# Kernel optimization log

Measured on AMD Instinct MI355X. Metric: run time of the kernel, lower is better.

## Reference

```python
import jax, jax.numpy as jnp
import numpy as np

N, L, G = 8192, 120, 256          # sentences, seq_len, bags
V, P = 80000, 202                 # word vocab, position vocab
WDIM, FDIM = 50, 5                # word_size, feature_size (width = 50+2*5 = 60)
D, C = 230, 53                    # cnn_layers, num_classes


def setup_inputs() -> dict:
    key = jax.random.key(0)
    ks = jax.random.split(key, 9)
    x = jax.random.randint(ks[0], (N, L), 0, V, dtype=jnp.int32)
    ldist = jax.random.randint(ks[1], (N, L), 0, P, dtype=jnp.int32)
    rdist = jax.random.randint(ks[2], (N, L), 0, P, dtype=jnp.int32)
    # cumulative bag boundaries: 256 equal bags of 32 sentences
    total_shape = (jnp.arange(G + 1, dtype=jnp.int32) * (N // G))
    Wv = jax.random.normal(ks[3], (V, WDIM), dtype=jnp.float32) * 0.1
    pf1 = jax.random.normal(ks[4], (P, FDIM), dtype=jnp.float32) * 0.1
    pf2 = jax.random.normal(ks[5], (P, FDIM), dtype=jnp.float32) * 0.1
    Wc = jax.random.normal(ks[6], (D, 1, 3, WDIM + 2 * FDIM), dtype=jnp.float32) * 0.05
    bc = jnp.zeros((D,), dtype=jnp.float32)
    Wr = jax.random.normal(ks[7], (C, D), dtype=jnp.float32) * 0.05
    br = jnp.zeros((C,), dtype=jnp.float32)
    return dict(x=x, ldist=ldist, rdist=rdist, total_shape=total_shape,
                Wv=Wv, pf1=pf1, pf2=pf2, Wc=Wc, bc=bc, Wr=Wr, br=br)


def reference(x, ldist, rdist, total_shape, Wv, pf1, pf2, Wc, bc, Wr, br):
    n = x.shape[0]
    g = total_shape.shape[0] - 1
    # getEmbeddings: concat word + two position embeddings -> (N, L, 60)
    emb = jnp.concatenate([Wv[x], pf1[ldist], pf2[rdist]], axis=-1)
    # Conv2d(1, D, (3, 60)), VALID -> (N, D, L-2, 1)
    conv = jax.lax.conv_general_dilated(
        emb[:, None, :, :], Wc, window_strides=(1, 1), padding='VALID',
        dimension_numbers=('NCHW', 'OIHW', 'NCHW')) + bc[None, :, None, None]
    # max over positions, squeeze; dropout is identity at eval; tanh
    sent = jnp.tanh(jnp.max(conv, axis=2)[:, :, 0])           # (N, D)
    e = sent @ Wr.T + br                                       # (N, C) batch_e
    # ragged per-bag softmax over sentences (per class), honoring total_shape
    seg = jnp.searchsorted(total_shape, jnp.arange(n), side='right') - 1  # (N,)
    m = jax.ops.segment_max(e, seg, num_segments=g)            # (G, C)
    ex = jnp.exp(e - m[seg])
    den = jax.ops.segment_sum(ex, seg, num_segments=g)
    alpha = ex / den[seg]                                      # (N, C)
    # bag_rep[g, c, :] = sum_i alpha[i, c] * sent[i, :]
    bag = jax.ops.segment_sum(alpha[:, :, None] * sent[:, None, :], seg,
                              num_segments=g)                  # (G, C, D)
    scores = jnp.einsum('gcd,kd->gck', bag, Wr) + br           # (G, C, C)
    probs = jax.nn.softmax(scores, axis=-1)
    return jnp.diagonal(probs, axis1=1, axis2=2)               # (G, C)
```

## Files before the change

kernel.cpp:

```cpp
#include <hip/hip_runtime.h>
#include <hip/hip_bf16.h>

typedef __bf16 bf16x8 __attribute__((ext_vector_type(8)));
typedef float f32x16 __attribute__((ext_vector_type(16)));
typedef unsigned short ushort_t;

#define NSENT 8192
#define LSEQ  120
#define GBAGS 256
#define WDIM_ 50
#define DFILT 230
#define NCLS  53
#define KSTEPS 12
#define BFRAG_ELEMS (24*256*8)
#define SPB 8
#define CH_STRIDE 2080
#define SENT_IMG  16640

#define OFF_BFRAG 0
#define OFF_WV64  196608
#define OFF_PF1B  (OFF_WV64 + 10240000)
#define OFF_PF2B  (OFF_PF1B + 2048)
#define OFF_SENT  (OFF_PF2B + 2048)
#define OFF_TAIL  (OFF_SENT + 7536640)

static __device__ __forceinline__ ushort_t f2bf(float f) {
    unsigned int u = __float_as_uint(f);
    unsigned int lsb = (u >> 16) & 1u;
    u += 0x7fffu + lsb;
    return (ushort_t)(u >> 16);
}

__global__ __launch_bounds__(256) void pcnn_prep_b(const float* __restrict__ Wc,
                                                   const float* __restrict__ pf1,
                                                   const float* __restrict__ pf2,
                                                   ushort_t* __restrict__ Bfrag,
                                                   ushort_t* __restrict__ pf1b,
                                                   ushort_t* __restrict__ pf2b) {
    int idx = blockIdx.x * 256 + threadIdx.x;
    if (idx < 1010) pf1b[idx] = f2bf(pf1[idx]);
    else if (idx < 2020) pf2b[idx - 1010] = f2bf(pf2[idx - 1010]);
    if (idx >= BFRAG_ELEMS) return;
    int c   = idx >> 11;
    int rem = idx & 2047;
    int d   = rem >> 3;
    int j   = rem & 7;
    int k   = c * 8 + j;
    int dh  = k >> 6;
    int w   = k & 63;
    float val = (d < DFILT && w < 60) ? Wc[(d * 3 + dh) * 60 + w] : 0.0f;
    Bfrag[idx] = f2bf(val);
}

__global__ __launch_bounds__(256) void pcnn_prep_wv(const float* __restrict__ Wv,
                                                    ushort_t* __restrict__ Wv64) {
    int idx = blockIdx.x * 256 + threadIdx.x;
    int r = idx >> 6, k = idx & 63;
    float val = (k < WDIM_) ? Wv[r * WDIM_ + k] : 0.0f;
    Wv64[idx] = f2bf(val);
}

__global__ __launch_bounds__(256) void pcnn_prep_tail(
    const int* __restrict__ x, const int* __restrict__ ld, const int* __restrict__ rd,
    const ushort_t* __restrict__ Wv64, const ushort_t* __restrict__ pf1b,
    const ushort_t* __restrict__ pf2b, ushort_t* __restrict__ TailT) {
    int idx = blockIdx.x * 256 + threadIdx.x;
    if (idx >= NSENT * LSEQ) return;
    int tok = x[idx], lp = ld[idx], rp = rd[idx];
    ushort_t u[16];
    *reinterpret_cast<unsigned int*>(&u[0]) =
        *reinterpret_cast<const unsigned int*>(Wv64 + (size_t)tok * 64 + 48);
    u[2] = pf1b[lp * 5 + 0]; u[3] = pf1b[lp * 5 + 1]; u[4] = pf1b[lp * 5 + 2];
    u[5] = pf1b[lp * 5 + 3]; u[6] = pf1b[lp * 5 + 4];
    u[7] = pf2b[rp * 5 + 0];
    u[8] = pf2b[rp * 5 + 1]; u[9] = pf2b[rp * 5 + 2];
    u[10] = pf2b[rp * 5 + 3]; u[11] = pf2b[rp * 5 + 4];
    u[12] = 0; u[13] = 0; u[14] = 0; u[15] = 0;
    uint4* dst = reinterpret_cast<uint4*>(TailT + idx * 16);
    dst[0] = *reinterpret_cast<const uint4*>(&u[0]);
    dst[1] = *reinterpret_cast<const uint4*>(&u[8]);
}

__global__ __launch_bounds__(256, 2) void pcnn_conv_sent(
    const int* __restrict__ x,
    const ushort_t* __restrict__ Wv64, const ushort_t* __restrict__ TailT,
    const ushort_t* __restrict__ Bfrag, const float* __restrict__ bc,
    float* __restrict__ sent) {

    __shared__ __align__(16) unsigned char semb[SENT_IMG];

    const int n0   = blockIdx.x * SPB;
    const int tid  = threadIdx.x;
    const int wv   = tid >> 6;
    const int lane = tid & 63;
    const int lhalf = lane >> 5;
    const int l31   = lane & 31;
    const int dcol0 = wv * 64 + l31;
    const int dcol1 = dcol0 + 32;

    const int srow = tid >> 1;
    const int sh   = tid & 1;
    const bool sact = (srow < LSEQ);

    bf16x8 Bf0[KSTEPS], Bf1[KSTEPS];
    #pragma unroll
    for (int ks = 0; ks < KSTEPS; ++ks) {
        int c = ks * 2 + lhalf;
        Bf0[ks] = *reinterpret_cast<const bf16x8*>(Bfrag + ((c * 256 + dcol0) << 3));
        Bf1[ks] = *reinterpret_cast<const bf16x8*>(Bfrag + ((c * 256 + dcol1) << 3));
    }
    const float bcv0 = (dcol0 < DFILT) ? bc[dcol0] : 0.0f;
    const float bcv1 = (dcol1 < DFILT) ? bc[dcol1] : 0.0f;

    int tokv[SPB];
    #pragma unroll
    for (int s = 0; s < SPB; ++s)
        tokv[s] = sact ? x[(n0 + s) * LSEQ + srow] : 0;

    if (tid < 80) {
        int c = tid / 10, r = 120 + tid % 10;
        *reinterpret_cast<uint4*>(semb + c * CH_STRIDE + r * 16) = uint4{0, 0, 0, 0};
    }

    uint4 r0, r1, r2, r3;
    if (sact) {
        int g = n0 * LSEQ + srow;
        const uint4* w = reinterpret_cast<const uint4*>(Wv64 + (size_t)tokv[0] * 64);
        if (sh == 0) { r0 = w[0]; r1 = w[1]; r2 = w[2]; r3 = w[3]; }
        else {
            r0 = w[4]; r1 = w[5];
            const uint4* t = reinterpret_cast<const uint4*>(TailT + (size_t)g * 16);
            r2 = t[0]; r3 = t[1];
        }
        unsigned char* p = semb + (sh * 4) * CH_STRIDE + srow * 16;
        *reinterpret_cast<uint4*>(p)                 = r0;
        *reinterpret_cast<uint4*>(p + CH_STRIDE)     = r1;
        *reinterpret_cast<uint4*>(p + 2 * CH_STRIDE) = r2;
        *reinterpret_cast<uint4*>(p + 3 * CH_STRIDE) = r3;
    }
    __syncthreads();

    #pragma unroll
    for (int s = 0; s < SPB; ++s) {
        if (s + 1 < SPB && sact) {
            int g = (n0 + s + 1) * LSEQ + srow;
            const uint4* w = reinterpret_cast<const uint4*>(Wv64 + (size_t)tokv[s + 1] * 64);
            if (sh == 0) { r0 = w[0]; r1 = w[1]; r2 = w[2]; r3 = w[3]; }
            else {
                r0 = w[4]; r1 = w[5];
                const uint4* t = reinterpret_cast<const uint4*>(TailT + (size_t)g * 16);
                r2 = t[0]; r3 = t[1];
            }
        }

        float dmax0 = -1e30f, dmax1 = -1e30f;
        #pragma unroll
        for (int tt = 0; tt < 4; ++tt) {
            f32x16 a0, a1;
            #pragma unroll
            for (int r = 0; r < 16; ++r) { a0[r] = 0.0f; a1[r] = 0.0f; }
            int trow = tt * 32 + l31;
            #pragma unroll
            for (int ks = 0; ks < KSTEPS; ++ks) {
                int dh = ks >> 2, q = ks & 3;
                int chunk = q * 2 + lhalf;
                int l = trow + dh;
                bf16x8 Af = *reinterpret_cast<const bf16x8*>(semb + chunk * CH_STRIDE + l * 16);
                a0 = __builtin_amdgcn_mfma_f32_32x32x16_bf16(Af, Bf0[ks], a0, 0, 0, 0);
                a1 = __builtin_amdgcn_mfma_f32_32x32x16_bf16(Af, Bf1[ks], a1, 0, 0, 0);
            }
            #pragma unroll
            for (int r = 0; r < 16; ++r) {
                int t = tt * 32 + (r & 3) + 8 * (r >> 2) + 4 * lhalf;
                bool valid = (tt < 3) || (t < LSEQ - 2);
                if (valid) { dmax0 = fmaxf(dmax0, a0[r]); dmax1 = fmaxf(dmax1, a1[r]); }
            }
        }
        dmax0 = fmaxf(dmax0, __shfl_xor(dmax0, 32));
        dmax1 = fmaxf(dmax1, __shfl_xor(dmax1, 32));
        if (lhalf == 0) {
            int n = n0 + s;
            if (dcol0 < DFILT) sent[n * DFILT + dcol0] = tanhf(dmax0 + bcv0);
            if (dcol1 < DFILT) sent[n * DFILT + dcol1] = tanhf(dmax1 + bcv1);
        }
        __syncthreads();

        if (s + 1 < SPB) {
            if (sact) {
                unsigned char* p = semb + (sh * 4) * CH_STRIDE + srow * 16;
                *reinterpret_cast<uint4*>(p)                 = r0;
                *reinterpret_cast<uint4*>(p + CH_STRIDE)     = r1;
                *reinterpret_cast<uint4*>(p + 2 * CH_STRIDE) = r2;
                *reinterpret_cast<uint4*>(p + 3 * CH_STRIDE) = r3;
            }
            __syncthreads();
        }
    }
}

#define MAXNS 32
#define CPAD 56
__global__ __launch_bounds__(256) void pcnn_bag(
    const float* __restrict__ sent, const float* __restrict__ Wr, const float* __restrict__ br,
    const int* __restrict__ tshape, float* __restrict__ out) {

    __shared__ float s_sent[MAXNS * DFILT];
    __shared__ float s_Wr[NCLS * DFILT];
    __shared__ float s_e[MAXNS * CPAD];
    __shared__ float s_alpha[MAXNS * CPAD];
    __shared__ float s_sc[NCLS * NCLS];
    __shared__ float s_br[CPAD];

    const int g = blockIdx.x;
    const int tid = threadIdx.x;
    int start = tshape[g], end = tshape[g + 1];
    int ns = end - start;
    if (ns > MAXNS) ns = MAXNS;

    {
        int n2 = ns * (DFILT / 2);
        const float2* src = reinterpret_cast<const float2*>(sent + start * DFILT);
        for (int idx = tid; idx < n2; idx += 256)
            reinterpret_cast<float2*>(s_sent)[idx] = src[idx];
        const float2* wsrc = reinterpret_cast<const float2*>(Wr);
        for (int idx = tid; idx < (NCLS * DFILT) / 2; idx += 256)
            reinterpret_cast<float2*>(s_Wr)[idx] = wsrc[idx];
        if (tid < NCLS) s_br[tid] = br[tid];
    }
    __syncthreads();

    if (tid < 224) {
        int i0 = tid / 14, c0 = tid % 14;
        float a00 = 0, a01 = 0, a02 = 0, a03 = 0;
        float a10 = 0, a11 = 0, a12 = 0, a13 = 0;
        const float* s0p = s_sent + (2 * i0) * DFILT;
        const float* s1p = s_sent + (2 * i0 + 1) * DFILT;
        const float* w0p = s_Wr + (4 * c0 + 0) * DFILT;
        const float* w1p = s_Wr + (4 * c0 + 1) * DFILT;
        const float* w2p = (4 * c0 + 2 < NCLS) ? s_Wr + (4 * c0 + 2) * DFILT : s_Wr;
        const float* w3p = (4 * c0 + 3 < NCLS) ? s_Wr + (4 * c0 + 3) * DFILT : s_Wr;
        for (int d = 0; d < DFILT; ++d) {
            float s0 = s0p[d], s1 = s1p[d];
            float w0 = w0p[d], w1 = w1p[d], w2 = w2p[d], w3 = w3p[d];
            a00 = fmaf(s0, w0, a00); a01 = fmaf(s0, w1, a01);
            a02 = fmaf(s0, w2, a02); a03 = fmaf(s0, w3, a03);
            a10 = fmaf(s1, w0, a10); a11 = fmaf(s1, w1, a11);
            a12 = fmaf(s1, w2, a12); a13 = fmaf(s1, w3, a13);
        }
        float av[2][4] = {{a00, a01, a02, a03}, {a10, a11, a12, a13}};
        #pragma unroll
        for (int ii = 0; ii < 2; ++ii) {
            int i = 2 * i0 + ii;
            #pragma unroll
            for (int jj = 0; jj < 4; ++jj) {
                int c = 4 * c0 + jj;
                if (i < ns && c < NCLS) s_e[i * CPAD + c] = av[ii][jj] + s_br[c];
            }
        }
    }
    __syncthreads();

    if (tid < NCLS) {
        int c = tid;
        float m = -1e30f;
        for (int i = 0; i < ns; ++i) m = fmaxf(m, s_e[i * CPAD + c]);
        float den = 0.0f;
        for (int i = 0; i < ns; ++i) {
            float ex = expf(s_e[i * CPAD + c] - m);
            s_alpha[i * CPAD + c] = ex;
            den += ex;
        }
        float inv = 1.0f / den;
        for (int i = 0; i < ns; ++i) s_alpha[i * CPAD + c] *= inv;
    }
    __syncthreads();

    for (int task = tid; task < NCLS * 14; task += 256) {
        int c = task / 14, k0 = (task % 14) * 4;
        float b0 = s_br[k0], b1 = (k0+1<NCLS)?s_br[k0+1]:0.f, b2 = (k0+2<NCLS)?s_br[k0+2]:0.f, b3 = (k0+3<NCLS)?s_br[k0+3]:0.f;
        float a0 = 0, a1 = 0, a2 = 0, a3 = 0;
        for (int i = 0; i < ns; ++i) {
            float al = s_alpha[i * CPAD + c];
            const float* ep = s_e + i * CPAD + k0;
            a0 = fmaf(al, ep[0] - b0, a0);
            a1 = fmaf(al, (k0+1<NCLS?ep[1]:0.f) - b1, a1);
            a2 = fmaf(al, (k0+2<NCLS?ep[2]:0.f) - b2, a2);
            a3 = fmaf(al, (k0+3<NCLS?ep[3]:0.f) - b3, a3);
        }
        if (k0 + 0 < NCLS) s_sc[c * NCLS + k0 + 0] = a0 + b0;
        if (k0 + 1 < NCLS) s_sc[c * NCLS + k0 + 1] = a1 + b1;
        if (k0 + 2 < NCLS) s_sc[c * NCLS + k0 + 2] = a2 + b2;
        if (k0 + 3 < NCLS) s_sc[c * NCLS + k0 + 3] = a3 + b3;
    }
    __syncthreads();

    if (tid < NCLS) {
        int c = tid;
        float m = -1e30f;
        for (int k = 0; k < NCLS; ++k) m = fmaxf(m, s_sc[c * NCLS + k]);
        float den = 0.0f;
        for (int k = 0; k < NCLS; ++k) den += expf(s_sc[c * NCLS + k] - m);
        out[g * NCLS + c] = expf(s_sc[c * NCLS + c] - m) / den;
    }
}

extern "C" void kernel_launch(void* const* d_in, const int* in_sizes, int n_in,
                              void* d_out, int out_size, void* d_ws, size_t ws_size,
                              hipStream_t stream) {
    const int*   x   = (const int*)d_in[0];
    const int*   ldi = (const int*)d_in[1];
    const int*   rdi = (const int*)d_in[2];
    const int*   ts  = (const int*)d_in[3];
    const float* Wv  = (const float*)d_in[4];
    const float* pf1 = (const float*)d_in[5];
    const float* pf2 = (const float*)d_in[6];
    const float* Wc  = (const float*)d_in[7];
    const float* bc  = (const float*)d_in[8];
    const float* Wr  = (const float*)d_in[9];
    const float* br  = (const float*)d_in[10];
    float* out = (float*)d_out;

    char* ws = (char*)d_ws;
    ushort_t* Bfrag = (ushort_t*)(ws + OFF_BFRAG);
    ushort_t* Wv64  = (ushort_t*)(ws + OFF_WV64);
    ushort_t* pf1b  = (ushort_t*)(ws + OFF_PF1B);
    ushort_t* pf2b  = (ushort_t*)(ws + OFF_PF2B);
    float*    sent  = (float*)(ws + OFF_SENT);
    ushort_t* TailT = (ushort_t*)(ws + OFF_TAIL);

    pcnn_prep_b<<<(BFRAG_ELEMS + 255) / 256, 256, 0, stream>>>(Wc, pf1, pf2, Bfrag, pf1b, pf2b);
    pcnn_prep_wv<<<(80000 * 64) / 256, 256, 0, stream>>>(Wv, Wv64);
    pcnn_prep_tail<<<(NSENT * LSEQ + 255) / 256, 256, 0, stream>>>(x, ldi, rdi, Wv64, pf1b, pf2b, TailT);
    pcnn_conv_sent<<<NSENT / SPB, 256, 0, stream>>>(x, Wv64, TailT, Bfrag, bc, sent);
    pcnn_bag<<<GBAGS, 256, 0, stream>>>(sent, Wr, br, ts, out);
}
```

Baseline: 160.8 us.

## Double-buffer sentence embeddings in LDS and drop word gather from tail prep

The conv kernel now keeps two LDS buffers, so it writes the next sentence's embedding into the idle buffer and needs only one barrier per sentence instead of two. The tail-prep kernel no longer gathers word-embedding columns 48-49. The conv kernel instead loads that part of the word row and ORs it with the position tail. Sentences per block drop from 8 to 4, which doubles the grid. In exchange, LDS per block doubles, which may lower occupancy, and each block reloads its B fragments more often relative to the work it does.

```diff
diff --git a/kernel.cpp b/kernel.cpp
--- a/kernel.cpp
+++ b/kernel.cpp
@@ -13,7 +13,7 @@
 #define NCLS  53
 #define KSTEPS 12
 #define BFRAG_ELEMS (24*256*8)
-#define SPB 8
+#define SPB 4
 #define CH_STRIDE 2080
 #define SENT_IMG  16640
 
@@ -61,15 +61,14 @@
 }
 
 __global__ __launch_bounds__(256) void pcnn_prep_tail(
-    const int* __restrict__ x, const int* __restrict__ ld, const int* __restrict__ rd,
-    const ushort_t* __restrict__ Wv64, const ushort_t* __restrict__ pf1b,
-    const ushort_t* __restrict__ pf2b, ushort_t* __restrict__ TailT) {
+    const int* __restrict__ ld, const int* __restrict__ rd,
+    const ushort_t* __restrict__ pf1b, const ushort_t* __restrict__ pf2b,
+    ushort_t* __restrict__ TailT) {
     int idx = blockIdx.x * 256 + threadIdx.x;
     if (idx >= NSENT * LSEQ) return;
-    int tok = x[idx], lp = ld[idx], rp = rd[idx];
+    int lp = ld[idx], rp = rd[idx];
     ushort_t u[16];
-    *reinterpret_cast<unsigned int*>(&u[0]) =
-        *reinterpret_cast<const unsigned int*>(Wv64 + (size_t)tok * 64 + 48);
+    u[0] = 0; u[1] = 0;
     u[2] = pf1b[lp * 5 + 0]; u[3] = pf1b[lp * 5 + 1]; u[4] = pf1b[lp * 5 + 2];
     u[5] = pf1b[lp * 5 + 3]; u[6] = pf1b[lp * 5 + 4];
     u[7] = pf2b[rp * 5 + 0];
@@ -87,7 +86,8 @@
     const ushort_t* __restrict__ Bfrag, const float* __restrict__ bc,
     float* __restrict__ sent) {
 
-    __shared__ __align__(16) unsigned char semb[SENT_IMG];
+    __shared__ __align__(16) unsigned char sembA[SENT_IMG];
+    __shared__ __align__(16) unsigned char sembB[SENT_IMG];
 
     const int n0   = blockIdx.x * SPB;
     const int tid  = threadIdx.x;
@@ -117,41 +117,54 @@
     for (int s = 0; s < SPB; ++s)
         tokv[s] = sact ? x[(n0 + s) * LSEQ + srow] : 0;
 
-    if (tid < 80) {
-        int c = tid / 10, r = 120 + tid % 10;
-        *reinterpret_cast<uint4*>(semb + c * CH_STRIDE + r * 16) = uint4{0, 0, 0, 0};
-    }
-
-    uint4 r0, r1, r2, r3;
+    if (tid < 160) {
+        int b = tid / 80, j = tid % 80;
+        int c = j / 10, r = 120 + j % 10;
+        unsigned char* base = (b == 0 ? sembA : sembB);
+        *reinterpret_cast<uint4*>(base + c * CH_STRIDE + r * 16) = uint4{0, 0, 0, 0};
+    }
+
+    uint4 r0, r1, r2, r3, r4;
     if (sact) {
-        int g = n0 * LSEQ + srow;
         const uint4* w = reinterpret_cast<const uint4*>(Wv64 + (size_t)tokv[0] * 64);
-        if (sh == 0) { r0 = w[0]; r1 = w[1]; r2 = w[2]; r3 = w[3]; }
+        if (sh == 0) { r0 = w[0]; r1 = w[1]; r2 = w[2]; r3 = w[3]; r4 = uint4{0,0,0,0}; }
         else {
-            r0 = w[4]; r1 = w[5];
-            const uint4* t = reinterpret_cast<const uint4*>(TailT + (size_t)g * 16);
-            r2 = t[0]; r3 = t[1];
-        }
-        unsigned char* p = semb + (sh * 4) * CH_STRIDE + srow * 16;
-        *reinterpret_cast<uint4*>(p)                 = r0;
-        *reinterpret_cast<uint4*>(p + CH_STRIDE)     = r1;
-        *reinterpret_cast<uint4*>(p + 2 * CH_STRIDE) = r2;
-        *reinterpret_cast<uint4*>(p + 3 * CH_STRIDE) = r3;
+            r0 = w[4]; r1 = w[5]; r2 = w[6];
+            const uint4* t = reinterpret_cast<const uint4*>(TailT + (size_t)(n0 * LSEQ + srow) * 16);
+            r3 = t[0]; r4 = t[1];
+        }
+        unsigned char* p = sembA + (sh * 4) * CH_STRIDE + srow * 16;
+        if (sh == 0) {
+            *reinterpret_cast<uint4*>(p)                 = r0;
+            *reinterpret_cast<uint4*>(p + CH_STRIDE)     = r1;
+            *reinterpret_cast<uint4*>(p + 2 * CH_STRIDE) = r2;
+            *reinterpret_cast<uint4*>(p + 3 * CH_STRIDE) = r3;
+        } else {
+            uint4 m; m.x = r2.x | r3.x; m.y = r2.y | r3.y; m.z = r2.z | r3.z; m.w = r2.w | r3.w;
+            *reinterpret_cast<uint4*>(p)                 = r0;
+            *reinterpret_cast<uint4*>(p + CH_STRIDE)     = r1;
+            *reinterpret_cast<uint4*>(p + 2 * CH_STRIDE) = m;
+            *reinterpret_cast<uint4*>(p + 3 * CH_STRIDE) = r4;
+        }
     }
     __syncthreads();
 
     #pragma unroll
     for (int s = 0; s < SPB; ++s) {
+        unsigned char* cur = (s & 1) ? sembB : sembA;
+        unsigned char* nxt = (s & 1) ? sembA : sembB;
+
         if (s + 1 < SPB && sact) {
-            int g = (n0 + s + 1) * LSEQ + srow;
             const uint4* w = reinterpret_cast<const uint4*>(Wv64 + (size_t)tokv[s + 1] * 64);
             if (sh == 0) { r0 = w[0]; r1 = w[1]; r2 = w[2]; r3 = w[3]; }
             else {
-                r0 = w[4]; r1 = w[5];
-                const uint4* t = reinterpret_cast<const uint4*>(TailT + (size_t)g * 16);
-                r2 = t[0]; r3 = t[1];
-            }
-        }
+                r0 = w[4]; r1 = w[5]; r2 = w[6];
+                const uint4* t = reinterpret_cast<const uint4*>(
+                    TailT + (size_t)((n0 + s + 1) * LSEQ + srow) * 16);
+                r3 = t[0]; r4 = t[1];
+            }
+        }
+        __builtin_amdgcn_sched_barrier(0);
 
         float dmax0 = -1e30f, dmax1 = -1e30f;
         #pragma unroll
@@ -165,7 +178,7 @@
                 int dh = ks >> 2, q = ks & 3;
                 int chunk = q * 2 + lhalf;
                 int l = trow + dh;
-                bf16x8 Af = *reinterpret_cast<const bf16x8*>(semb + chunk * CH_STRIDE + l * 16);
+                bf16x8 Af = *reinterpret_cast<const bf16x8*>(cur + chunk * CH_STRIDE + l * 16);
                 a0 = __builtin_amdgcn_mfma_f32_32x32x16_bf16(Af, Bf0[ks], a0, 0, 0, 0);
                 a1 = __builtin_amdgcn_mfma_f32_32x32x16_bf16(Af, Bf1[ks], a1, 0, 0, 0);
             }
@@ -183,18 +196,23 @@
             if (dcol0 < DFILT) sent[n * DFILT + dcol0] = tanhf(dmax0 + bcv0);
             if (dcol1 < DFILT) sent[n * DFILT + dcol1] = tanhf(dmax1 + bcv1);
         }
-        __syncthreads();
-
-        if (s + 1 < SPB) {
-            if (sact) {
-                unsigned char* p = semb + (sh * 4) * CH_STRIDE + srow * 16;
+
+        if (s + 1 < SPB && sact) {
+            unsigned char* p = nxt + (sh * 4) * CH_STRIDE + srow * 16;
+            if (sh == 0) {
                 *reinterpret_cast<uint4*>(p)                 = r0;
                 *reinterpret_cast<uint4*>(p + CH_STRIDE)     = r1;
                 *reinterpret_cast<uint4*>(p + 2 * CH_STRIDE) = r2;
                 *reinterpret_cast<uint4*>(p + 3 * CH_STRIDE) = r3;
-            }
-            __syncthreads();
-        }
+            } else {
+                uint4 m; m.x = r2.x | r3.x; m.y = r2.y | r3.y; m.z = r2.z | r3.z; m.w = r2.w | r3.w;
+                *reinterpret_cast<uint4*>(p)                 = r0;
+                *reinterpret_cast<uint4*>(p + CH_STRIDE)     = r1;
+                *reinterpret_cast<uint4*>(p + 2 * CH_STRIDE) = m;
+                *reinterpret_cast<uint4*>(p + 3 * CH_STRIDE) = r4;
+            }
+        }
+        __syncthreads();
     }
 }
 
@@ -330,7 +348,7 @@
 
     pcnn_prep_b<<<(BFRAG_ELEMS + 255) / 256, 256, 0, stream>>>(Wc, pf1, pf2, Bfrag, pf1b, pf2b);
     pcnn_prep_wv<<<(80000 * 64) / 256, 256, 0, stream>>>(Wv, Wv64);
-    pcnn_prep_tail<<<(NSENT * LSEQ + 255) / 256, 256, 0, stream>>>(x, ldi, rdi, Wv64, pf1b, pf2b, TailT);
+    pcnn_prep_tail<<<(NSENT * LSEQ + 255) / 256, 256, 0, stream>>>(ldi, rdi, pf1b, pf2b, TailT);
     pcnn_conv_sent<<<NSENT / SPB, 256, 0, stream>>>(x, Wv64, TailT, Bfrag, bc, sent);
     pcnn_bag<<<GBAGS, 256, 0, stream>>>(sent, Wr, br, ts, out);
 }
```

Result: no change. 158.5 us (-1.4%).
